# Optimization experiments

Measured on AMD Instinct MI355X. Metric: run time of the kernel, lower is better.

Reference implementation:

```python
import jax, jax.numpy as jnp
import numpy as np
from jax import lax

B, DIM, H, W = 8, 192, 128, 128
K = 7            # kernel_size
STRIDE = 1
PAD = 3          # kernel_size // 2
RED = 4          # reduction
HID = DIM // RED # 48
EPS = 1e-5       # BatchNorm eps


def setup_inputs() -> dict:
    key = jax.random.key(0)
    ks = jax.random.split(key, 4)
    return {
        "x": jax.random.normal(ks[0], (B, DIM, H, W), dtype=jnp.float32),
        # conv1: 1x1, no bias -> [out=HID, in=DIM]
        "w1": jax.random.normal(ks[1], (HID, DIM), dtype=jnp.float32) * 0.05,
        # BatchNorm2d(HID) eval-mode params / running stats
        "bn_gamma": jnp.ones((HID,), jnp.float32),
        "bn_beta": jnp.zeros((HID,), jnp.float32),
        "bn_mean": jnp.zeros((HID,), jnp.float32),
        "bn_var": jnp.ones((HID,), jnp.float32),
        # conv2: 1x1 -> [out=DIM*K*K, in=HID], with bias
        "w2": jax.random.normal(ks[2], (DIM * K * K, HID), dtype=jnp.float32) * 0.05,
        "b2": jnp.zeros((DIM * K * K,), jnp.float32),
        # depthwise output bias (self.bias)
        "bias": jax.random.normal(ks[3], (DIM,), dtype=jnp.float32) * 0.05,
    }


def reference(x, w1, bn_gamma, bn_beta, bn_mean, bn_var, w2, b2, bias):
    b, c, h, w = x.shape
    # SE-style weight generation: pool -> 1x1 conv -> BN -> ReLU -> 1x1 conv
    pooled = x.mean(axis=(2, 3))                          # [b, c]
    y = jnp.einsum('bc,oc->bo', pooled, w1)               # [b, HID]
    y = (y - bn_mean) * lax.rsqrt(bn_var + EPS) * bn_gamma + bn_beta
    y = jax.nn.relu(y)
    wdyn = jnp.einsum('bh,oh->bo', y, w2) + b2            # [b, c*K*K]
    wdyn = wdyn.reshape(b, c, K, K)                       # per-sample depthwise kernels

    # per-sample depthwise conv (equiv. to groups=b*dim batch-folded trick)
    def dw(xi, wi):  # xi: [c,h,w], wi: [c,K,K]
        return lax.conv_general_dilated(
            xi[None], wi[:, None],              # [1,c,h,w], [c,1,K,K] (OIHW)
            window_strides=(STRIDE, STRIDE),
            padding=[(PAD, PAD), (PAD, PAD)],
            feature_group_count=c)[0]

    out = jax.vmap(dw)(x, wdyn) + bias[None, :, None, None]
    return out
```

## Files before the change

### kernel.cpp

```cpp
#include <hip/hip_runtime.h>

#define BATCH 8
#define DIM 192
#define HH 128
#define WW 128
#define KS 7
#define PAD 3
#define HID 48
#define KK 49
#define BN_EPS 1e-5f
#define WSTR 52

#define TILE_H 64
#define SROWS (TILE_H + KS - 1)
#define NSLOT (SROWS * (WW / 4))
#define NTILE (HH / TILE_H)
#define RPT   8

static_assert(NSLOT % 64 == 0, "staging guard must be wave-uniform");

__global__ __launch_bounds__(256) void pool_kernel(const float* __restrict__ x,
                                                   float* __restrict__ pooled) {
    const int bc = blockIdx.x;
    const float4* p = (const float4*)(x + (size_t)bc * HH * WW);
    const int t = threadIdx.x;
    float s = 0.f;
#pragma unroll
    for (int i = 0; i < 16; ++i) {
        float4 v = p[t + i * 256];
        s += (v.x + v.y) + (v.z + v.w);
    }
#pragma unroll
    for (int off = 32; off > 0; off >>= 1) s += __shfl_down(s, off, 64);
    __shared__ float wsum[4];
    const int wave = t >> 6, lane = t & 63;
    if (lane == 0) wsum[wave] = s;
    __syncthreads();
    if (t == 0) {
        float tot = (wsum[0] + wsum[1]) + (wsum[2] + wsum[3]);
        pooled[bc] = tot * (1.0f / (HH * WW));
    }
}

__global__ __launch_bounds__(64) void wgen_full_kernel(
        const float* __restrict__ pooled,
        const float* __restrict__ w1,
        const float* __restrict__ gamma,
        const float* __restrict__ beta,
        const float* __restrict__ mean,
        const float* __restrict__ var,
        const float* __restrict__ w2,
        const float* __restrict__ b2,
        float* __restrict__ wdyn) {
    __shared__ float y_s[HID];
    const int bc = blockIdx.x;
    const int b = bc / DIM, c = bc % DIM;
    const int t = threadIdx.x;
    if (t < HID) {
        const float4* pr = (const float4*)(pooled + b * DIM);
        const float4* wr = (const float4*)(w1 + (size_t)t * DIM);
        float acc = 0.f;
#pragma unroll
        for (int j = 0; j < DIM / 4; ++j) {
            float4 pv = pr[j], wv = wr[j];
            acc += pv.x * wv.x + pv.y * wv.y + pv.z * wv.z + pv.w * wv.w;
        }
        float yv = (acc - mean[t]) * rsqrtf(var[t] + BN_EPS) * gamma[t] + beta[t];
        y_s[t] = yv > 0.f ? yv : 0.f;
    }
    __syncthreads();
    if (t < KK) {
        const int o = c * KK + t;
        const float4* w2r = (const float4*)(w2 + (size_t)o * HID);
        float acc = b2[o];
#pragma unroll
        for (int j = 0; j < HID / 4; ++j) {
            float4 wv = w2r[j];
            acc += y_s[4 * j] * wv.x + y_s[4 * j + 1] * wv.y +
                   y_s[4 * j + 2] * wv.z + y_s[4 * j + 3] * wv.w;
        }
        wdyn[(size_t)bc * WSTR + t] = acc;
    }
}

__global__ __launch_bounds__(256) void dwconv_hoisted_kernel(
        const float* __restrict__ x,
        const float* __restrict__ wdyn,
        const float* __restrict__ bias,
        float* __restrict__ out) {
    __shared__ float smem[SROWS][WW];
    __shared__ float wk_s[KK];
    const int tile = blockIdx.x & (NTILE - 1);
    const int bc = blockIdx.x >> 1;
    const int c = bc % DIM;
    const int t = threadIdx.x;
    const int r0 = tile * TILE_H;

    const int slo = (tile == 0) ? PAD * (WW / 4) : 0;
    const int shi = (tile == NTILE - 1) ? (SROWS - PAD) * (WW / 4) : NSLOT;
    const float* xbase = x + (size_t)bc * HH * WW + (ptrdiff_t)(r0 - PAD) * WW;

#pragma unroll
    for (int i = 0; i < (NSLOT + 255) / 256; ++i) {
        const int s = t + i * 256;
        if (s < NSLOT) {
            int sc = s;
            if (sc < slo) sc = slo;
            if (sc >= shi) sc = shi - 1;
            __builtin_amdgcn_global_load_lds(
                (const __attribute__((address_space(1))) void*)(xbase + (size_t)sc * 4),
                (__attribute__((address_space(3))) void*)((float*)smem + (size_t)s * 4),
                16, 0, 0);
        }
    }

    if (t < KK) wk_s[t] = wdyn[(size_t)bc * WSTR + t];
    __syncthreads();

    if (t < 96) {
        const int zslot = (tile ? (SROWS - PAD) * (WW / 4) : 0) + t;
        ((float4*)smem)[zslot] = make_float4(0.f, 0.f, 0.f, 0.f);
    }
    __syncthreads();

    float wreg[KK];
#pragma unroll
    for (int i = 0; i < KK; ++i) wreg[i] = wk_s[i];
    const float bv = bias[c];

    const int c4 = t & 31;
    const int strip = t >> 5;
    const int sbase = strip * RPT;
    float* outp = out + (size_t)bc * HH * WW + (size_t)(r0 + sbase) * WW + c4 * 4;

    float acc[7][4];
#pragma unroll
    for (int i = 0; i < 7; ++i)
        acc[i][0] = acc[i][1] = acc[i][2] = acc[i][3] = 0.f;

#pragma unroll
    for (int ir = 0; ir < RPT + KS - 1; ++ir) {
        const float4* row4 = (const float4*)&smem[sbase + ir][0];
        const float4 f1 = row4[c4];
        float4 f0 = make_float4(0.f, 0.f, 0.f, 0.f);
        float4 f2 = make_float4(0.f, 0.f, 0.f, 0.f);
        if (c4 > 0)  f0 = row4[c4 - 1];
        if (c4 < 31) f2 = row4[c4 + 1];
        const float v[12] = {f0.x, f0.y, f0.z, f0.w,
                             f1.x, f1.y, f1.z, f1.w,
                             f2.x, f2.y, f2.z, f2.w};
#pragma unroll
        for (int ky = 0; ky < KS; ++ky) {
            const int o = ir - ky;
            if (o >= 0 && o < RPT) {
                float* a = acc[o % 7];
#pragma unroll
                for (int kx = 0; kx < KS; ++kx) {
                    const float wv = wreg[ky * KS + kx];
                    a[0] += wv * v[1 + kx];
                    a[1] += wv * v[2 + kx];
                    a[2] += wv * v[3 + kx];
                    a[3] += wv * v[4 + kx];
                }
            }
        }
        if (ir >= KS - 1) {
            float* a = acc[(ir - (KS - 1)) % 7];
            float4 o4 = make_float4(a[0] + bv, a[1] + bv, a[2] + bv, a[3] + bv);
            *((float4*)(outp + (size_t)(ir - (KS - 1)) * WW)) = o4;
            a[0] = a[1] = a[2] = a[3] = 0.f;
        }
    }
}

extern "C" void kernel_launch(void* const* d_in, const int* in_sizes, int n_in,
                              void* d_out, int out_size, void* d_ws, size_t ws_size,
                              hipStream_t stream) {
    const float* x     = (const float*)d_in[0];
    const float* w1    = (const float*)d_in[1];
    const float* gamma = (const float*)d_in[2];
    const float* beta  = (const float*)d_in[3];
    const float* mean  = (const float*)d_in[4];
    const float* var   = (const float*)d_in[5];
    const float* w2    = (const float*)d_in[6];
    const float* b2    = (const float*)d_in[7];
    const float* bias  = (const float*)d_in[8];
    float* out = (float*)d_out;

    float* pooled = (float*)d_ws;
    float* wdyn   = pooled + BATCH * DIM;

    pool_kernel<<<BATCH * DIM, 256, 0, stream>>>(x, pooled);
    wgen_full_kernel<<<BATCH * DIM, 64, 0, stream>>>(
        pooled, w1, gamma, beta, mean, var, w2, b2, wdyn);
    dwconv_hoisted_kernel<<<BATCH * DIM * NTILE, 256, 0, stream>>>(
        x, wdyn, bias, out);
}
```

Baseline: 226.2 us.

## Split depthwise conv into single-wave 16-row bands without block barriers

The depthwise conv is re-gridded from 256-thread blocks covering 64 rows to 64-thread single-wave blocks covering 16-row bands. With one wave per block, both __syncthreads are replaced by an explicit vmcnt wait on the async global-to-LDS loads. The per-channel weights now come straight from global memory as float4 loads instead of being staged through shared memory. The aim is to remove barrier stalls and give the scheduler more, smaller blocks, at the cost of more halo rows re-read per output row.

```diff
diff --git a/kernel.cpp b/kernel.cpp
--- a/kernel.cpp
+++ b/kernel.cpp
@@ -11,13 +11,13 @@
 #define BN_EPS 1e-5f
 #define WSTR 52
 
-#define TILE_H 64
-#define SROWS (TILE_H + KS - 1)
+#define BAND_H 16
+#define SROWS (BAND_H + KS - 1)
 #define NSLOT (SROWS * (WW / 4))
-#define NTILE (HH / TILE_H)
+#define NBAND (HH / BAND_H)
 #define RPT   8
 
-static_assert(NSLOT % 64 == 0, "staging guard must be wave-uniform");
+static_assert(NSLOT % 64 == 0, "staging must keep all 64 lanes active");
 
 __global__ __launch_bounds__(256) void pool_kernel(const float* __restrict__ x,
                                                    float* __restrict__ pooled) {
@@ -83,50 +83,59 @@
     }
 }
 
-__global__ __launch_bounds__(256) void dwconv_hoisted_kernel(
+__global__ __launch_bounds__(64) void dwconv_wave_kernel(
         const float* __restrict__ x,
         const float* __restrict__ wdyn,
         const float* __restrict__ bias,
         float* __restrict__ out) {
     __shared__ float smem[SROWS][WW];
-    __shared__ float wk_s[KK];
-    const int tile = blockIdx.x & (NTILE - 1);
-    const int bc = blockIdx.x >> 1;
+    const int band = blockIdx.x & (NBAND - 1);
+    const int bc = blockIdx.x >> 3;
     const int c = bc % DIM;
     const int t = threadIdx.x;
-    const int r0 = tile * TILE_H;
-
-    const int slo = (tile == 0) ? PAD * (WW / 4) : 0;
-    const int shi = (tile == NTILE - 1) ? (SROWS - PAD) * (WW / 4) : NSLOT;
+    const int r0 = band * BAND_H;
+
+    const float4* wrow = (const float4*)(wdyn + (size_t)bc * WSTR);
+    float4 w4[13];
+#pragma unroll
+    for (int i = 0; i < 13; ++i) w4[i] = wrow[i];
+
+    const int slo = (band == 0) ? PAD * (WW / 4) : 0;
+    const int shi = (band == NBAND - 1) ? (SROWS - PAD) * (WW / 4) : NSLOT;
     const float* xbase = x + (size_t)bc * HH * WW + (ptrdiff_t)(r0 - PAD) * WW;
 
 #pragma unroll
-    for (int i = 0; i < (NSLOT + 255) / 256; ++i) {
-        const int s = t + i * 256;
-        if (s < NSLOT) {
-            int sc = s;
-            if (sc < slo) sc = slo;
-            if (sc >= shi) sc = shi - 1;
-            __builtin_amdgcn_global_load_lds(
-                (const __attribute__((address_space(1))) void*)(xbase + (size_t)sc * 4),
-                (__attribute__((address_space(3))) void*)((float*)smem + (size_t)s * 4),
-                16, 0, 0);
-        }
-    }
-
-    if (t < KK) wk_s[t] = wdyn[(size_t)bc * WSTR + t];
-    __syncthreads();
-
-    if (t < 96) {
-        const int zslot = (tile ? (SROWS - PAD) * (WW / 4) : 0) + t;
-        ((float4*)smem)[zslot] = make_float4(0.f, 0.f, 0.f, 0.f);
-    }
-    __syncthreads();
+    for (int i = 0; i < NSLOT / 64; ++i) {
+        const int s = t + i * 64;
+        int sc = s;
+        if (sc < slo) sc = slo;
+        if (sc >= shi) sc = shi - 1;
+        __builtin_amdgcn_global_load_lds(
+            (const __attribute__((address_space(1))) void*)(xbase + (size_t)sc * 4),
+            (__attribute__((address_space(3))) void*)((float*)smem + (size_t)s * 4),
+            16, 0, 0);
+    }
 
     float wreg[KK];
 #pragma unroll
-    for (int i = 0; i < KK; ++i) wreg[i] = wk_s[i];
+    for (int i = 0; i < 12; ++i) {
+        wreg[4 * i + 0] = w4[i].x;
+        wreg[4 * i + 1] = w4[i].y;
+        wreg[4 * i + 2] = w4[i].z;
+        wreg[4 * i + 3] = w4[i].w;
+    }
+    wreg[48] = w4[12].x;
     const float bv = bias[c];
+
+    asm volatile("s_waitcnt vmcnt(0)" ::: "memory");
+
+    if (band == 0) {
+        ((float4*)smem)[t] = make_float4(0.f, 0.f, 0.f, 0.f);
+        if (t < 32) ((float4*)smem)[64 + t] = make_float4(0.f, 0.f, 0.f, 0.f);
+    } else if (band == NBAND - 1) {
+        ((float4*)smem)[608 + t] = make_float4(0.f, 0.f, 0.f, 0.f);
+        if (t < 32) ((float4*)smem)[672 + t] = make_float4(0.f, 0.f, 0.f, 0.f);
+    }
 
     const int c4 = t & 31;
     const int strip = t >> 5;
@@ -193,6 +202,6 @@
     pool_kernel<<<BATCH * DIM, 256, 0, stream>>>(x, pooled);
     wgen_full_kernel<<<BATCH * DIM, 64, 0, stream>>>(
         pooled, w1, gamma, beta, mean, var, w2, b2, wdyn);
-    dwconv_hoisted_kernel<<<BATCH * DIM * NTILE, 256, 0, stream>>>(
+    dwconv_wave_kernel<<<BATCH * DIM * NBAND, 64, 0, stream>>>(
         x, wdyn, bias, out);
 }
```

After: 222.5 us. No clear change (-1.6%).
